# Performance work log

Hardware: AMD Instinct MI355X
Metric: run time of the kernel (lower is better)

Reference implementation:

```python
import jax, jax.numpy as jnp
import numpy as np

B, T_FRAMES, T_TOKENS = 2048, 8192, 1024
MAX_DUR = 16.0


def setup_inputs() -> dict:
    key = jax.random.key(0)
    k1, k2, k3, k4 = jax.random.split(key, 4)
    frame_scalar = jax.random.normal(k1, (B, T_FRAMES), dtype=jnp.float32)
    # float durations as the duration predictor would emit (hard mode rounds them)
    duration = jax.random.uniform(k2, (B, T_TOKENS), dtype=jnp.float32) * MAX_DUR
    frame_scalar_len = jax.random.randint(k3, (B,), 1, T_FRAMES + 1, dtype=jnp.int32)
    duration_len = jax.random.randint(k4, (B,), 1, T_TOKENS + 1, dtype=jnp.int32)
    return {
        "frame_scalar": frame_scalar,
        "duration": duration,
        "frame_scalar_len": frame_scalar_len,
        "duration_len": duration_len,
    }


def reference(frame_scalar, duration, frame_scalar_len, duration_len):
    """Hard-mode duration-based frame->token scalar averaging (FastSpeech2).

    Equivalent to FastSpeech2Decoder.proc_duration (hard, min_frame_num=0,
    max_frame_num=None, reduction_factor=1) followed by
    average_scalar_by_duration with len_regulation_type='hard', vectorized via
    prefix sums instead of nested Python loops.
    """
    Bb, Tt = duration.shape
    # proc_duration: round + clamp to [0, inf)
    dur = jnp.clip(jnp.round(duration), 0.0, None)  # [B, T_tok]
    # zero out tokens beyond duration_len (loop only runs j < duration_len[i])
    tok_valid = jnp.arange(Tt, dtype=jnp.int32)[None, :] < duration_len[:, None]
    dur = jnp.where(tok_valid, dur, 0.0)
    # cumulative end positions, clipped at frame_scalar_len exactly like the
    # running-cursor clipping d = min(d, L - cursor) in the torch loop
    flen = frame_scalar_len.astype(jnp.float32)[:, None]  # [B,1]
    ends_f = jnp.minimum(jnp.cumsum(dur, axis=1), flen)    # [B, T_tok]
    starts_f = jnp.concatenate([jnp.zeros((Bb, 1), dtype=ends_f.dtype), ends_f[:, :-1]], axis=1)
    d = ends_f - starts_f  # effective (clipped) segment lengths
    # segment sums via exclusive prefix sum of frame_scalar: [B, T_frames+1]
    cfs = jnp.concatenate(
        [jnp.zeros((Bb, 1), dtype=jnp.float32), jnp.cumsum(frame_scalar, axis=1)], axis=1
    )
    e_idx = ends_f.astype(jnp.int32)
    s_idx = starts_f.astype(jnp.int32)
    seg_sum = jnp.take_along_axis(cfs, e_idx, axis=1) - jnp.take_along_axis(cfs, s_idx, axis=1)
    token_scalar = jnp.where(d > 0, seg_sum / jnp.maximum(d, 1.0), 0.0)  # [B, T_tok]
    return token_scalar, duration_len
```

## Files before the change

kernel.cpp:

```cpp
#include <hip/hip_runtime.h>


namespace {
constexpr int TT = 1024;
constexpr int TF = 8192;
constexpr int NT = 512;
constexpr int NW = NT / 64;

__device__ __forceinline__ float wave_scan_incl(float x) {
    float f = x;
    {
        int t_ = __builtin_amdgcn_update_dpp(0, __float_as_int(f), 0x111, 0xf, 0xf, false);
        f += __int_as_float(t_);
    }
    {
        int t_ = __builtin_amdgcn_update_dpp(0, __float_as_int(f), 0x112, 0xf, 0xf, false);
        f += __int_as_float(t_);
    }
    {
        int t_ = __builtin_amdgcn_update_dpp(0, __float_as_int(f), 0x114, 0xf, 0xf, false);
        f += __int_as_float(t_);
    }
    {
        int t_ = __builtin_amdgcn_update_dpp(0, __float_as_int(f), 0x118, 0xf, 0xf, false);
        f += __int_as_float(t_);
    }
    {
        int t_ = __builtin_amdgcn_update_dpp(0, __float_as_int(f), 0x142, 0xa, 0xf, false);
        f += __int_as_float(t_);
    }
    {
        int t_ = __builtin_amdgcn_update_dpp(0, __float_as_int(f), 0x143, 0xc, 0xf, false);
        f += __int_as_float(t_);
    }
    return f;
}

__device__ __forceinline__ float readlane63(float x) {
    return __int_as_float(__builtin_amdgcn_readlane(__float_as_int(x), 63));
}
}

__global__ __launch_bounds__(NT, 6) void fs2_avg_kernel(
    const float* __restrict__ frame_scalar,
    const float* __restrict__ duration,
    const int* __restrict__ frame_scalar_len,
    const int* __restrict__ duration_len,
    float* __restrict__ out,
    int n_rows)
{
    __shared__ alignas(16) float s_S[TF];
    __shared__ alignas(16) float s_wA[NW];
    __shared__ alignas(16) float s_wF[NW];

    const int b = blockIdx.x;
    const int t = threadIdx.x;
    const int lane = t & 63;
    const int wid = t >> 6;

    const int dlen = duration_len[b];
    const int flen_i = frame_scalar_len[b];
    const float flen = (float)flen_i;

    const float* frow = frame_scalar + (size_t)b * TF;

    if (t == 0) out[(size_t)n_rows * TT + b] = (float)dlen;

    const int j0 = t * 2;
    float2 d2 = (j0 < dlen)
        ? *reinterpret_cast<const float2*>(duration + (size_t)b * TT + j0)
        : make_float2(0.f, 0.f);

    const int qb = 256 * wid + lane;
    float4 v0 = make_float4(0.f, 0.f, 0.f, 0.f);
    float4 v1 = v0, v2 = v0, v3 = v0;
    if (4 * (qb)       < flen_i) v0 = *reinterpret_cast<const float4*>(frow + 4 * (qb));
    if (4 * (qb + 64)  < flen_i) v1 = *reinterpret_cast<const float4*>(frow + 4 * (qb + 64));
    if (4 * (qb + 128) < flen_i) v2 = *reinterpret_cast<const float4*>(frow + 4 * (qb + 128));
    if (4 * (qb + 192) < flen_i) v3 = *reinterpret_cast<const float4*>(frow + 4 * (qb + 192));

    float d0 = fmaxf(rintf(d2.x), 0.0f);
    float d1 = fmaxf(rintf(d2.y), 0.0f);
    if (j0 + 1 >= dlen) d1 = 0.0f;
    const float c0 = d0, c1 = c0 + d1;

    float p0[4], p1[4], p2[4], p3[4];
    p0[0] = v0.x; p0[1] = p0[0] + v0.y; p0[2] = p0[1] + v0.z; p0[3] = p0[2] + v0.w;
    p1[0] = v1.x; p1[1] = p1[0] + v1.y; p1[2] = p1[1] + v1.z; p1[3] = p1[2] + v1.w;
    p2[0] = v2.x; p2[1] = p2[0] + v2.y; p2[2] = p2[1] + v2.z; p2[3] = p2[2] + v2.w;
    p3[0] = v3.x; p3[1] = p3[0] + v3.y; p3[2] = p3[1] + v3.z; p3[3] = p3[2] + v3.w;

    const float ws  = wave_scan_incl(c1);
    const float f0s = wave_scan_incl(p0[3]);
    const float f1s = wave_scan_incl(p1[3]);
    const float f2s = wave_scan_incl(p2[3]);
    const float f3s = wave_scan_incl(p3[3]);

    const float T0 = readlane63(f0s);
    const float T1 = readlane63(f1s);
    const float T2 = readlane63(f2s);
    const float T3 = readlane63(f3s);
    const float C1 = T0, C2 = T0 + T1, C3 = C2 + T2;
    const float Fw = C3 + T3;

    if (lane == 63) { s_wA[wid] = ws; s_wF[wid] = Fw; }

    __syncthreads();

    const float4 wA0 = *reinterpret_cast<const float4*>(&s_wA[0]);
    const float4 wA1 = *reinterpret_cast<const float4*>(&s_wA[4]);
    float base = ws - c1;
    base += (wid > 0) ? wA0.x : 0.f;
    base += (wid > 1) ? wA0.y : 0.f;
    base += (wid > 2) ? wA0.z : 0.f;
    base += (wid > 3) ? wA0.w : 0.f;
    base += (wid > 4) ? wA1.x : 0.f;
    base += (wid > 5) ? wA1.y : 0.f;
    base += (wid > 6) ? wA1.z : 0.f;

    const float4 wF0 = *reinterpret_cast<const float4*>(&s_wF[0]);
    const float4 wF1 = *reinterpret_cast<const float4*>(&s_wF[4]);
    float FB = 0.0f;
    FB += (wid > 0) ? wF0.x : 0.f;
    FB += (wid > 1) ? wF0.y : 0.f;
    FB += (wid > 2) ? wF0.z : 0.f;
    FB += (wid > 3) ? wF0.w : 0.f;
    FB += (wid > 4) ? wF1.x : 0.f;
    FB += (wid > 5) ? wF1.y : 0.f;
    FB += (wid > 6) ? wF1.z : 0.f;

    {
        const float eb0 = FB      + (f0s - p0[3]);
        const float eb1 = FB + C1 + (f1s - p1[3]);
        const float eb2 = FB + C2 + (f2s - p2[3]);
        const float eb3 = FB + C3 + (f3s - p3[3]);
        *reinterpret_cast<float4*>(&s_S[4 * (qb)]) =
            make_float4(eb0 + p0[0], eb0 + p0[1], eb0 + p0[2], eb0 + p0[3]);
        *reinterpret_cast<float4*>(&s_S[4 * (qb + 64)]) =
            make_float4(eb1 + p1[0], eb1 + p1[1], eb1 + p1[2], eb1 + p1[3]);
        *reinterpret_cast<float4*>(&s_S[4 * (qb + 128)]) =
            make_float4(eb2 + p2[0], eb2 + p2[1], eb2 + p2[2], eb2 + p2[3]);
        *reinterpret_cast<float4*>(&s_S[4 * (qb + 192)]) =
            make_float4(eb3 + p3[0], eb3 + p3[1], eb3 + p3[2], eb3 + p3[3]);
    }

    __syncthreads();

    const float sprev0 = (j0 == 0) ? 0.0f : fminf(base, flen);
    const float e0 = fminf(base + c0, flen);
    const float e1 = fminf(base + c1, flen);

    const int si = (int)sprev0;
    const int mi = (int)e0;
    const int ei = (int)e1;

    float o0 = 0.0f, o1 = 0.0f;
    if (ei > si) {
        const float Gs = (si == 0) ? 0.0f : s_S[si - 1];
        const float Gm = (mi == 0) ? 0.0f : s_S[mi - 1];
        const float Ge = s_S[ei - 1];
        o0 = (mi > si) ? (Gm - Gs) * __builtin_amdgcn_rcpf(e0 - sprev0) : 0.0f;
        o1 = (ei > mi) ? (Ge - Gm) * __builtin_amdgcn_rcpf(e1 - e0) : 0.0f;
    }

    *reinterpret_cast<float2*>(out + (size_t)b * TT + j0) = make_float2(o0, o1);
}

extern "C" void kernel_launch(void* const* d_in, const int* in_sizes, int n_in,
                              void* d_out, int out_size, void* d_ws, size_t ws_size,
                              hipStream_t stream) {
    const float* frame_scalar     = (const float*)d_in[0];
    const float* duration         = (const float*)d_in[1];
    const int*   frame_scalar_len = (const int*)d_in[2];
    const int*   duration_len     = (const int*)d_in[3];
    float* out = (float*)d_out;
    const int B = in_sizes[2];
    fs2_avg_kernel<<<B, NT, 0, stream>>>(frame_scalar, duration, frame_scalar_len,
                                         duration_len, out, B);
}
```

Measured before the change: 14.31 us.

## Load only frames covered by total duration, defer wave-offset addition to lookup

Computes the block-wide duration scan first and uses the clipped total duration to bound the frame_scalar loads, skipping frames that no token segment can reference. The cross-wave frame prefix offsets are no longer folded into shared memory; they are added at lookup time for the three gathered indices. This serializes the frame load behind the duration scan and barrier, which reduces load overlap. Launch bounds are also raised to 8 blocks per CU.

Result: faster. 12.98 us (median of 2 runs) (-9.3%).

```diff
diff --git a/kernel.cpp b/kernel.cpp
--- a/kernel.cpp
+++ b/kernel.cpp
@@ -41,7 +41,7 @@
 }
 }
 
-__global__ __launch_bounds__(NT, 6) void fs2_avg_kernel(
+__global__ __launch_bounds__(NT, 8) void fs2_avg_kernel(
     const float* __restrict__ frame_scalar,
     const float* __restrict__ duration,
     const int* __restrict__ frame_scalar_len,
@@ -70,40 +70,13 @@
     float2 d2 = (j0 < dlen)
         ? *reinterpret_cast<const float2*>(duration + (size_t)b * TT + j0)
         : make_float2(0.f, 0.f);
-
-    const int qb = 256 * wid + lane;
-    float4 v0 = make_float4(0.f, 0.f, 0.f, 0.f);
-    float4 v1 = v0, v2 = v0, v3 = v0;
-    if (4 * (qb)       < flen_i) v0 = *reinterpret_cast<const float4*>(frow + 4 * (qb));
-    if (4 * (qb + 64)  < flen_i) v1 = *reinterpret_cast<const float4*>(frow + 4 * (qb + 64));
-    if (4 * (qb + 128) < flen_i) v2 = *reinterpret_cast<const float4*>(frow + 4 * (qb + 128));
-    if (4 * (qb + 192) < flen_i) v3 = *reinterpret_cast<const float4*>(frow + 4 * (qb + 192));
-
     float d0 = fmaxf(rintf(d2.x), 0.0f);
     float d1 = fmaxf(rintf(d2.y), 0.0f);
     if (j0 + 1 >= dlen) d1 = 0.0f;
     const float c0 = d0, c1 = c0 + d1;
 
-    float p0[4], p1[4], p2[4], p3[4];
-    p0[0] = v0.x; p0[1] = p0[0] + v0.y; p0[2] = p0[1] + v0.z; p0[3] = p0[2] + v0.w;
-    p1[0] = v1.x; p1[1] = p1[0] + v1.y; p1[2] = p1[1] + v1.z; p1[3] = p1[2] + v1.w;
-    p2[0] = v2.x; p2[1] = p2[0] + v2.y; p2[2] = p2[1] + v2.z; p2[3] = p2[2] + v2.w;
-    p3[0] = v3.x; p3[1] = p3[0] + v3.y; p3[2] = p3[1] + v3.z; p3[3] = p3[2] + v3.w;
-
-    const float ws  = wave_scan_incl(c1);
-    const float f0s = wave_scan_incl(p0[3]);
-    const float f1s = wave_scan_incl(p1[3]);
-    const float f2s = wave_scan_incl(p2[3]);
-    const float f3s = wave_scan_incl(p3[3]);
-
-    const float T0 = readlane63(f0s);
-    const float T1 = readlane63(f1s);
-    const float T2 = readlane63(f2s);
-    const float T3 = readlane63(f3s);
-    const float C1 = T0, C2 = T0 + T1, C3 = C2 + T2;
-    const float Fw = C3 + T3;
-
-    if (lane == 63) { s_wA[wid] = ws; s_wF[wid] = Fw; }
+    const float ws = wave_scan_incl(c1);
+    if (lane == 63) s_wA[wid] = ws;
 
     __syncthreads();
 
@@ -118,22 +91,48 @@
     base += (wid > 5) ? wA1.y : 0.f;
     base += (wid > 6) ? wA1.z : 0.f;
 
-    const float4 wF0 = *reinterpret_cast<const float4*>(&s_wF[0]);
-    const float4 wF1 = *reinterpret_cast<const float4*>(&s_wF[4]);
-    float FB = 0.0f;
-    FB += (wid > 0) ? wF0.x : 0.f;
-    FB += (wid > 1) ? wF0.y : 0.f;
-    FB += (wid > 2) ? wF0.z : 0.f;
-    FB += (wid > 3) ? wF0.w : 0.f;
-    FB += (wid > 4) ? wF1.x : 0.f;
-    FB += (wid > 5) ? wF1.y : 0.f;
-    FB += (wid > 6) ? wF1.z : 0.f;
+    const float total = wA0.x + wA0.y + wA0.z + wA0.w
+                      + wA1.x + wA1.y + wA1.z + wA1.w;
+    const int Fneed_i = (int)fminf(total, flen);
+
+    const int qb = 256 * wid + lane;
+    float4 v0 = make_float4(0.f, 0.f, 0.f, 0.f);
+    float4 v1 = v0, v2 = v0, v3 = v0;
+    if (4 * (qb)       < Fneed_i) v0 = *reinterpret_cast<const float4*>(frow + 4 * (qb));
+    if (4 * (qb + 64)  < Fneed_i) v1 = *reinterpret_cast<const float4*>(frow + 4 * (qb + 64));
+    if (4 * (qb + 128) < Fneed_i) v2 = *reinterpret_cast<const float4*>(frow + 4 * (qb + 128));
+    if (4 * (qb + 192) < Fneed_i) v3 = *reinterpret_cast<const float4*>(frow + 4 * (qb + 192));
+
+    const float sprev0 = (j0 == 0) ? 0.0f : fminf(base, flen);
+    const float e0 = fminf(base + c0, flen);
+    const float e1 = fminf(base + c1, flen);
+    const int si = (int)sprev0;
+    const int mi = (int)e0;
+    const int ei = (int)e1;
+
+    float p0[4], p1[4], p2[4], p3[4];
+    p0[0] = v0.x; p0[1] = p0[0] + v0.y; p0[2] = p0[1] + v0.z; p0[3] = p0[2] + v0.w;
+    p1[0] = v1.x; p1[1] = p1[0] + v1.y; p1[2] = p1[1] + v1.z; p1[3] = p1[2] + v1.w;
+    p2[0] = v2.x; p2[1] = p2[0] + v2.y; p2[2] = p2[1] + v2.z; p2[3] = p2[2] + v2.w;
+    p3[0] = v3.x; p3[1] = p3[0] + v3.y; p3[2] = p3[1] + v3.z; p3[3] = p3[2] + v3.w;
+
+    const float f0s = wave_scan_incl(p0[3]);
+    const float f1s = wave_scan_incl(p1[3]);
+    const float f2s = wave_scan_incl(p2[3]);
+    const float f3s = wave_scan_incl(p3[3]);
+
+    const float T0 = readlane63(f0s);
+    const float T1 = readlane63(f1s);
+    const float T2 = readlane63(f2s);
+    const float T3 = readlane63(f3s);
+    const float Cc1 = T0, Cc2 = T0 + T1, Cc3 = Cc2 + T2;
+    const float Fw = Cc3 + T3;
 
     {
-        const float eb0 = FB      + (f0s - p0[3]);
-        const float eb1 = FB + C1 + (f1s - p1[3]);
-        const float eb2 = FB + C2 + (f2s - p2[3]);
-        const float eb3 = FB + C3 + (f3s - p3[3]);
+        const float eb0 =       (f0s - p0[3]);
+        const float eb1 = Cc1 + (f1s - p1[3]);
+        const float eb2 = Cc2 + (f2s - p2[3]);
+        const float eb3 = Cc3 + (f3s - p3[3]);
         *reinterpret_cast<float4*>(&s_S[4 * (qb)]) =
             make_float4(eb0 + p0[0], eb0 + p0[1], eb0 + p0[2], eb0 + p0[3]);
         *reinterpret_cast<float4*>(&s_S[4 * (qb + 64)]) =
@@ -143,22 +142,31 @@
         *reinterpret_cast<float4*>(&s_S[4 * (qb + 192)]) =
             make_float4(eb3 + p3[0], eb3 + p3[1], eb3 + p3[2], eb3 + p3[3]);
     }
+    if (lane == 63) s_wF[wid] = Fw;
 
     __syncthreads();
 
-    const float sprev0 = (j0 == 0) ? 0.0f : fminf(base, flen);
-    const float e0 = fminf(base + c0, flen);
-    const float e1 = fminf(base + c1, flen);
-
-    const int si = (int)sprev0;
-    const int mi = (int)e0;
-    const int ei = (int)e1;
+    const float4 wF0 = *reinterpret_cast<const float4*>(&s_wF[0]);
+    const float4 wF1 = *reinterpret_cast<const float4*>(&s_wF[4]);
 
     float o0 = 0.0f, o1 = 0.0f;
     if (ei > si) {
-        const float Gs = (si == 0) ? 0.0f : s_S[si - 1];
-        const float Gm = (mi == 0) ? 0.0f : s_S[mi - 1];
-        const float Ge = s_S[ei - 1];
+        auto G = [&](int idx) -> float {
+            const int i = idx - 1;
+            const int w = i >> 10;
+            float s = s_S[i];
+            s += (w > 0) ? wF0.x : 0.f;
+            s += (w > 1) ? wF0.y : 0.f;
+            s += (w > 2) ? wF0.z : 0.f;
+            s += (w > 3) ? wF0.w : 0.f;
+            s += (w > 4) ? wF1.x : 0.f;
+            s += (w > 5) ? wF1.y : 0.f;
+            s += (w > 6) ? wF1.z : 0.f;
+            return s;
+        };
+        const float Gs = (si == 0) ? 0.0f : G(si);
+        const float Gm = (mi == 0) ? 0.0f : G(mi);
+        const float Ge = G(ei);
         o0 = (mi > si) ? (Gm - Gs) * __builtin_amdgcn_rcpf(e0 - sprev0) : 0.0f;
         o1 = (ei > mi) ? (Ge - Gm) * __builtin_amdgcn_rcpf(e1 - e0) : 0.0f;
     }
```
